# Kernel tuning notes

Measured on AMD Instinct MI355X. Metric: run time of the kernel, lower is better.

The kernel has to match this reference:

```python
import jax, jax.numpy as jnp
import numpy as np

IMG = 448; P = 16; C = 3; D = 512; DC = 8; DS = 4
NH = IMG // P            # 28 patches per side
NPATCH = NH * NH         # 784
PDIM = C * P * P         # 768
BATCH = 32
EPS = 1e-5


def setup_inputs() -> dict:
    key = jax.random.key(0)
    ks = jax.random.split(key, 10)
    def lin(k, fan_in, shape):
        bound = 1.0 / np.sqrt(fan_in)
        return jax.random.uniform(k, shape, jnp.float32, -bound, bound)
    return {
        "images": jax.random.normal(ks[0], (BATCH, C, IMG, IMG), jnp.float32),
        "W_patch": lin(ks[1], PDIM, (PDIM, D)),
        "b_patch": jnp.zeros((D,), jnp.float32),
        "pos_embed": jax.random.normal(ks[2], (1, NPATCH, D), jnp.float32) * 0.02,
        "W_coord": lin(ks[3], D, (D, DC)),
        "b_coord": jnp.zeros((DC,), jnp.float32),
        "W_spinor": lin(ks[4], D, (D, DS)),
        "b_spinor": jnp.zeros((DS,), jnp.float32),
        "W_embed": lin(ks[5], DC, (DC, D)),
        "b_embed": jnp.zeros((D,), jnp.float32),
        "ln_gamma": jnp.ones((D,), jnp.float32),
        "ln_beta": jnp.zeros((D,), jnp.float32),
        "W_out": lin(ks[6], D, (D, D)),
        "b_out": jnp.zeros((D,), jnp.float32),
    }


def reference(images, W_patch, b_patch, pos_embed, W_coord, b_coord,
              W_spinor, b_spinor, W_embed, b_embed,
              ln_gamma, ln_beta, W_out, b_out):
    B = images.shape[0]
    # patchify == F.unfold(kernel=stride=P).transpose(1,2):
    # patches[b, bh*NH+bw, c*P*P + i*P + j] = images[b, c, bh*P+i, bw*P+j]
    patches = images.reshape(B, C, NH, P, NH, P)
    patches = patches.transpose(0, 2, 4, 1, 3, 5).reshape(B, NPATCH, PDIM)
    # patch embed + positional embedding  -> (B, NPATCH, D)
    x = patches @ W_patch + b_patch + pos_embed
    # manifold projection: coords (B,N,DC), spinor (B,N,DS)
    coords = x @ W_coord + b_coord
    spinor = x @ W_spinor + b_spinor
    # K0 scalar bilinear: psi^T psi -> (B, N)
    K0 = jnp.sum(spinor * spinor, axis=-1)
    # embed back from manifold coords -> (B, N, D)
    x_manifold = coords @ W_embed + b_embed
    # K0-modulated remix + residual
    x_enh = x_manifold * K0[..., None] + x
    # output projection: LayerNorm -> Linear
    mu = jnp.mean(x_enh, axis=-1, keepdims=True)
    var = jnp.mean(jnp.square(x_enh - mu), axis=-1, keepdims=True)
    x_norm = (x_enh - mu) * jax.lax.rsqrt(var + EPS) * ln_gamma + ln_beta
    return x_norm @ W_out + b_out
```

## Files before the change

### kernel.cpp

```cpp
#include <hip/hip_runtime.h>
#include <hip/hip_bf16.h>
#include <stdint.h>


typedef __bf16 bf16_t;
typedef bf16_t bf16x8 __attribute__((ext_vector_type(8)));
typedef bf16_t bf16x4 __attribute__((ext_vector_type(4)));
typedef float  f32x4  __attribute__((ext_vector_type(4)));

#define IMG     448
#define PSZ     16
#define NHP     28
#define NPATCH  784
#define PDIM    768
#define DMODEL  512
#define MROWS   25088

__device__ __forceinline__ void gload16(void* lds, const void* g) {
  __builtin_amdgcn_global_load_lds(
      (__attribute__((address_space(1))) void*)(uintptr_t)g,
      (__attribute__((address_space(3))) void*)lds,
      16, 0, 0);
}

__global__ __launch_bounds__(256) void transpose_to_bf16(
    const float* __restrict__ src, bf16_t* __restrict__ dst, int K, int N)
{
  __shared__ float t[64][65];
  const int tx = threadIdx.x;
  const int ty = threadIdx.y;
  const int bx = blockIdx.x * 64;
  const int by = blockIdx.y * 64;
  #pragma unroll
  for (int r = ty; r < 64; r += 4)
    t[r][tx] = src[(size_t)(by + r) * N + (bx + tx)];
  __syncthreads();
  #pragma unroll
  for (int r = ty; r < 64; r += 4)
    dst[(size_t)(bx + r) * K + (by + tx)] = (bf16_t)t[tx][r];
}

__global__ __launch_bounds__(256) void manifold_prep(
    const float* __restrict__ Wc, const float* __restrict__ Ws,
    bf16_t* __restrict__ Wcsg)
{
  const int idx = blockIdx.x * 256 + threadIdx.x;
  if (idx < 8192) {
    const int r = idx >> 9, n = idx & 511;
    float v = 0.f;
    if (r < 8)       v = Wc[n * 8 + r];
    else if (r < 12) v = Ws[n * 4 + (r - 8)];
    Wcsg[idx] = (bf16_t)v;
  }
}

__global__ __launch_bounds__(256) void gemm1_fused(
    const float* __restrict__ images, const bf16_t* __restrict__ BT,
    const float* __restrict__ bias, const float* __restrict__ pos,
    bf16_t* __restrict__ outp)
{
  __shared__ bf16_t As[64 * 64];
  __shared__ bf16_t Bs[128 * 64];
  constexpr int NT = PDIM / 64;

  const int tid  = threadIdx.x;
  const int orig = blockIdx.x;
  const int wg   = (orig & 7) * 196 + (orig >> 3);
  const int n0   = (wg & 3) * 128;
  const int m0   = (wg >> 2) * 64;

  const int wave = tid >> 6, lane = tid & 63;

  const int r_loc = tid >> 2;
  const int seg   = tid & 3;
  {
  }
  const int m  = m0 + r_loc;
  const int b  = m / NPATCH;
  const int p  = m - b * NPATCH;
  const int ph = p / NHP;
  const int pw = p - ph * NHP;
  const float* abase = images + ((size_t)(b * 3) * IMG + ph * PSZ) * IMG + pw * PSZ;
  bf16_t* aw0 = As + r_loc * 64 + (((2 * seg)     ^ (r_loc & 7)) * 8);
  bf16_t* aw1 = As + r_loc * 64 + (((2 * seg + 1) ^ (r_loc & 7)) * 8);

  const int ra = lane >> 3;
  const int ca = (lane & 7) ^ ra;
  const bf16_t* bg = BT + (size_t)(n0 + wave * 8 + ra) * PDIM + ca * 8;
  bf16_t* bl0 = Bs + (wave * 8) * 64;
  bf16_t* bl1 = Bs + (wave * 8 + 32) * 64;
  bf16_t* bl2 = Bs + (wave * 8 + 64) * 64;
  bf16_t* bl3 = Bs + (wave * 8 + 96) * 64;

  const int wm = (wave >> 1) * 32;
  const int wn = (wave & 1) * 64;
  const int lr = lane & 15;
  const int lt = lane >> 4;

  f32x4 acc[2][4] = {};

  for (int t = 0; t < NT; ++t) {
    const int k0 = t * 64;
    const float* asrc = abase + (size_t)(t >> 2) * (IMG * IMG)
                              + ((t & 3) * 4 + seg) * IMG;
    const float4 v0 = *(const float4*)(asrc + 0);
    const float4 v1 = *(const float4*)(asrc + 4);
    const float4 v2 = *(const float4*)(asrc + 8);
    const float4 v3 = *(const float4*)(asrc + 12);

    __syncthreads();
    bf16x8 w0, w1;
    w0[0] = (bf16_t)v0.x; w0[1] = (bf16_t)v0.y; w0[2] = (bf16_t)v0.z; w0[3] = (bf16_t)v0.w;
    w0[4] = (bf16_t)v1.x; w0[5] = (bf16_t)v1.y; w0[6] = (bf16_t)v1.z; w0[7] = (bf16_t)v1.w;
    w1[0] = (bf16_t)v2.x; w1[1] = (bf16_t)v2.y; w1[2] = (bf16_t)v2.z; w1[3] = (bf16_t)v2.w;
    w1[4] = (bf16_t)v3.x; w1[5] = (bf16_t)v3.y; w1[6] = (bf16_t)v3.z; w1[7] = (bf16_t)v3.w;
    *(bf16x8*)aw0 = w0;
    *(bf16x8*)aw1 = w1;
    gload16(bl0, bg + k0);
    gload16(bl1, bg + 32 * PDIM + k0);
    gload16(bl2, bg + 64 * PDIM + k0);
    gload16(bl3, bg + 96 * PDIM + k0);
    __syncthreads();

    #pragma unroll
    for (int ks = 0; ks < 2; ++ks) {
      const int c = ks * 4 + lt;
      bf16x8 af[2], bfr[4];
      #pragma unroll
      for (int i = 0; i < 2; ++i) {
        const int row = wm + i * 16 + lr;
        af[i] = *(const bf16x8*)&As[row * 64 + ((c ^ (row & 7)) * 8)];
      }
      #pragma unroll
      for (int j = 0; j < 4; ++j) {
        const int row = wn + j * 16 + lr;
        bfr[j] = *(const bf16x8*)&Bs[row * 64 + ((c ^ (row & 7)) * 8)];
      }
      #pragma unroll
      for (int i = 0; i < 2; ++i)
        #pragma unroll
        for (int j = 0; j < 4; ++j)
          acc[i][j] = __builtin_amdgcn_mfma_f32_16x16x32_bf16(af[i], bfr[j], acc[i][j], 0, 0, 0);
    }
  }

  const int q4 = lt << 2;
  const int colb = n0 + wn;
  #pragma unroll
  for (int i = 0; i < 2; ++i) {
    #pragma unroll
    for (int r = 0; r < 4; ++r) {
      const int mm = m0 + wm + i * 16 + q4 + r;
      const int pp = mm % NPATCH;
      const float* pe = pos + (size_t)pp * DMODEL;
      bf16_t* orow = outp + (size_t)mm * DMODEL;
      #pragma unroll
      for (int j = 0; j < 4; ++j) {
        const int nn = colb + j * 16 + lr;
        orow[nn] = (bf16_t)(acc[i][j][r] + bias[nn] + pe[nn]);
      }
    }
  }
}

__global__ __launch_bounds__(256) void gemm2_v5(
    const bf16_t* __restrict__ A, const bf16_t* __restrict__ BT,
    const float* __restrict__ bias, float* __restrict__ outp)
{
  __shared__ bf16_t As[64 * 64];
  __shared__ bf16_t Bs[128 * 64];
  constexpr int KDIM = DMODEL;
  constexpr int NT = KDIM / 64;

  const int tid  = threadIdx.x;
  const int orig = blockIdx.x;
  const int wg   = (orig & 7) * 196 + (orig >> 3);
  const int n0   = (wg & 3) * 128;
  const int m0   = (wg >> 2) * 64;

  const int wave = tid >> 6, lane = tid & 63;
  const int ra = lane >> 3;
  const int ca = (lane & 7) ^ ra;
  const bf16_t* ag = A  + (size_t)(m0 + wave * 8 + ra) * KDIM + ca * 8;
  const bf16_t* bg = BT + (size_t)(n0 + wave * 8 + ra) * KDIM + ca * 8;
  bf16_t* al0 = As + (wave * 8) * 64;
  bf16_t* al1 = As + (wave * 8 + 32) * 64;
  bf16_t* bl0 = Bs + (wave * 8) * 64;
  bf16_t* bl1 = Bs + (wave * 8 + 32) * 64;
  bf16_t* bl2 = Bs + (wave * 8 + 64) * 64;
  bf16_t* bl3 = Bs + (wave * 8 + 96) * 64;

  const int wm = (wave >> 1) * 32;
  const int wn = (wave & 1) * 64;
  const int lr = lane & 15;
  const int lt = lane >> 4;

  f32x4 acc[2][4] = {};

  for (int t = 0; t < NT; ++t) {
    const int k0 = t * 64;
    __syncthreads();
    gload16(al0, ag + k0);
    gload16(al1, ag + 32 * KDIM + k0);
    gload16(bl0, bg + k0);
    gload16(bl1, bg + 32 * KDIM + k0);
    gload16(bl2, bg + 64 * KDIM + k0);
    gload16(bl3, bg + 96 * KDIM + k0);
    __syncthreads();

    #pragma unroll
    for (int ks = 0; ks < 2; ++ks) {
      const int c = ks * 4 + lt;
      bf16x8 af[2], bfr[4];
      #pragma unroll
      for (int i = 0; i < 2; ++i) {
        const int row = wm + i * 16 + lr;
        af[i] = *(const bf16x8*)&As[row * 64 + ((c ^ (row & 7)) * 8)];
      }
      #pragma unroll
      for (int j = 0; j < 4; ++j) {
        const int row = wn + j * 16 + lr;
        bfr[j] = *(const bf16x8*)&Bs[row * 64 + ((c ^ (row & 7)) * 8)];
      }
      #pragma unroll
      for (int i = 0; i < 2; ++i)
        #pragma unroll
        for (int j = 0; j < 4; ++j)
          acc[i][j] = __builtin_amdgcn_mfma_f32_16x16x32_bf16(af[i], bfr[j], acc[i][j], 0, 0, 0);
    }
  }

  const int q4 = lt << 2;
  const int colb = n0 + wn;
  #pragma unroll
  for (int i = 0; i < 2; ++i) {
    #pragma unroll
    for (int r = 0; r < 4; ++r) {
      const int mm = m0 + wm + i * 16 + q4 + r;
      float* orow = outp + (size_t)mm * DMODEL;
      #pragma unroll
      for (int j = 0; j < 4; ++j) {
        const int nn = colb + j * 16 + lr;
        orow[nn] = acc[i][j][r] + bias[nn];
      }
    }
  }
}

__global__ __launch_bounds__(64) void manifold_v5(
    bf16_t* __restrict__ x, const bf16_t* __restrict__ Wcsg,
    const float* __restrict__ b_coord, const float* __restrict__ b_spinor,
    const float* __restrict__ We, const float* __restrict__ be,
    const float* __restrict__ gamma, const float* __restrict__ beta)
{
  __shared__ float cbuf[16][12];

  const int lane = threadIdx.x;
  const int lr   = lane & 15;
  const int lk   = (lane >> 4) << 3;
  const int q4   = (lane >> 4) << 2;
  const int m0w  = blockIdx.x * 16;

  float bbv[4];
  #pragma unroll
  for (int r = 0; r < 4; ++r) {
    if (q4 == 0)      bbv[r] = b_coord[r];
    else if (q4 == 4) bbv[r] = b_coord[4 + r];
    else if (q4 == 8) bbv[r] = b_spinor[r];
    else              bbv[r] = 0.f;
  }

  const bf16_t* xrow = x + (size_t)(m0w + lr) * DMODEL + lk;
  const bf16_t* wrow = Wcsg + lr * DMODEL + lk;
  f32x4 acc1 = {0.f, 0.f, 0.f, 0.f};
  #pragma unroll
  for (int ks = 0; ks < 16; ++ks) {
    const bf16x8 bf = *(const bf16x8*)(xrow + ks * 32);
    const bf16x8 wf = *(const bf16x8*)(wrow + ks * 32);
    acc1 = __builtin_amdgcn_mfma_f32_16x16x32_bf16(wf, bf, acc1, 0, 0, 0);
  }
  float sv[4];
  #pragma unroll
  for (int r = 0; r < 4; ++r) sv[r] = acc1[r] + bbv[r];

  if (q4 == 8) {
    cbuf[lr][8] = sv[0] * sv[0] + sv[1] * sv[1] + sv[2] * sv[2] + sv[3] * sv[3];
  } else if (q4 == 0 || q4 == 4) {
    f32x4 st = {sv[0], sv[1], sv[2], sv[3]};
    *(f32x4*)&cbuf[lr][q4] = st;
  }
  __syncthreads();

  const int n0 = lane * 8;
  f32x4 wlo[8], whi[8];
  #pragma unroll
  for (int dc = 0; dc < 8; ++dc) {
    wlo[dc] = *(const f32x4*)&We[dc * DMODEL + n0];
    whi[dc] = *(const f32x4*)&We[dc * DMODEL + n0 + 4];
  }
  const f32x4 beL = *(const f32x4*)&be[n0];
  const f32x4 beH = *(const f32x4*)&be[n0 + 4];
  const f32x4 gL  = *(const f32x4*)&gamma[n0];
  const f32x4 gH  = *(const f32x4*)&gamma[n0 + 4];
  const f32x4 btL = *(const f32x4*)&beta[n0];
  const f32x4 btH = *(const f32x4*)&beta[n0 + 4];

  #pragma unroll 2
  for (int rr = 0; rr < 16; ++rr) {
    const size_t row = (size_t)m0w + rr;
    const bf16x8 xv = *(const bf16x8*)(x + row * DMODEL + n0);
    const f32x4 c0 = *(const f32x4*)&cbuf[rr][0];
    const f32x4 c1 = *(const f32x4*)&cbuf[rr][4];
    const float k0 = cbuf[rr][8];

    float v[8];
    float s1 = 0.f, s2 = 0.f;
    #pragma unroll
    for (int e = 0; e < 4; ++e) {
      float xm = beL[e];
      #pragma unroll
      for (int dc = 0; dc < 4; ++dc) xm += c0[dc] * wlo[dc][e];
      #pragma unroll
      for (int dc = 0; dc < 4; ++dc) xm += c1[dc] * wlo[4 + dc][e];
      const float vv = xm * k0 + (float)xv[e];
      v[e] = vv; s1 += vv; s2 += vv * vv;
    }
    #pragma unroll
    for (int e = 0; e < 4; ++e) {
      float xm = beH[e];
      #pragma unroll
      for (int dc = 0; dc < 4; ++dc) xm += c0[dc] * whi[dc][e];
      #pragma unroll
      for (int dc = 0; dc < 4; ++dc) xm += c1[dc] * whi[4 + dc][e];
      const float vv = xm * k0 + (float)xv[4 + e];
      v[4 + e] = vv; s1 += vv; s2 += vv * vv;
    }

    #pragma unroll
    for (int off = 1; off <= 32; off <<= 1) {
      s1 += __shfl_xor(s1, off, 64);
      s2 += __shfl_xor(s2, off, 64);
    }
    const float mu  = s1 * (1.f / 512.f);
    const float var = s2 * (1.f / 512.f) - mu * mu;
    const float rs  = rsqrtf(var + 1e-5f);

    bf16x8 o;
    #pragma unroll
    for (int e = 0; e < 4; ++e) {
      o[e]     = (bf16_t)((v[e]     - mu) * rs * gL[e] + btL[e]);
      o[4 + e] = (bf16_t)((v[4 + e] - mu) * rs * gH[e] + btH[e]);
    }
    *(bf16x8*)(x + row * DMODEL + n0) = o;
  }
}

extern "C" void kernel_launch(void* const* d_in, const int* in_sizes, int n_in,
                              void* d_out, int out_size, void* d_ws, size_t ws_size,
                              hipStream_t stream)
{
  const float* images    = (const float*)d_in[0];
  const float* W_patch   = (const float*)d_in[1];
  const float* b_patch   = (const float*)d_in[2];
  const float* pos_embed = (const float*)d_in[3];
  const float* W_coord   = (const float*)d_in[4];
  const float* b_coord   = (const float*)d_in[5];
  const float* W_spinor  = (const float*)d_in[6];
  const float* b_spinor  = (const float*)d_in[7];
  const float* W_embed   = (const float*)d_in[8];
  const float* b_embed   = (const float*)d_in[9];
  const float* ln_gamma  = (const float*)d_in[10];
  const float* ln_beta   = (const float*)d_in[11];
  const float* W_out     = (const float*)d_in[12];
  const float* b_out     = (const float*)d_in[13];
  float* out = (float*)d_out;

  const size_t SZ_X    = (size_t)MROWS * DMODEL * 2;
  const size_t SZ_WPT  = (size_t)DMODEL * PDIM * 2;
  const size_t SZ_WOT  = (size_t)DMODEL * DMODEL * 2;

  char* ws = (char*)d_ws;
  char* p  = ws;
  bf16_t* x    = (bf16_t*)p;   p += SZ_X;
  bf16_t* WpT  = (bf16_t*)p;   p += SZ_WPT;
  bf16_t* WoT  = (bf16_t*)p;   p += SZ_WOT;
  bf16_t* Wcsg = (bf16_t*)p;

  hipLaunchKernelGGL(transpose_to_bf16, dim3(8, 12), dim3(64, 4), 0, stream,
                     W_patch, WpT, PDIM, DMODEL);
  hipLaunchKernelGGL(transpose_to_bf16, dim3(8, 8), dim3(64, 4), 0, stream,
                     W_out, WoT, DMODEL, DMODEL);
  hipLaunchKernelGGL(manifold_prep, dim3(32), dim3(256), 0, stream,
                     W_coord, W_spinor, Wcsg);

  hipLaunchKernelGGL(gemm1_fused, dim3(1568), dim3(256), 0, stream,
                     images, WpT, b_patch, pos_embed, x);

  hipLaunchKernelGGL(manifold_v5, dim3(MROWS / 16), dim3(64), 0, stream,
                     x, Wcsg, b_coord, b_spinor, W_embed, b_embed, ln_gamma, ln_beta);

  hipLaunchKernelGGL(gemm2_v5, dim3(1568), dim3(256), 0, stream,
                     x, WoT, b_out, out);
}
```

Baseline: 123.3 us.

## Split patchify into separate kernel and triple-buffer GEMM LDS loads

Moves the fp32-to-bf16 patch extraction out of the first GEMM into a standalone patchify kernel that writes a bf16 patch matrix. Both GEMMs then share one templated kernel with a three-stage LDS ring buffer of async global-to-LDS loads, two tiles in flight, waited on with explicit vmcnt counts, so memory latency overlaps MFMA work. The cost is an extra pass that writes and rereads a large intermediate patch buffer, plus triple the LDS per block, which may lower occupancy.

```diff
diff --git a/kernel.cpp b/kernel.cpp
--- a/kernel.cpp
+++ b/kernel.cpp
@@ -54,14 +54,47 @@
   }
 }
 
-__global__ __launch_bounds__(256) void gemm1_fused(
-    const float* __restrict__ images, const bf16_t* __restrict__ BT,
+__global__ __launch_bounds__(256) void patchify_bf16(
+    const float* __restrict__ images, bf16_t* __restrict__ Apat)
+{
+  __shared__ bf16_t t[16][456];
+  const int tid = threadIdx.x;
+  const int bid = blockIdx.x;
+  const int b = bid / 84, rem = bid % 84;
+  const int c = rem / 28, ph = rem % 28;
+  const float* src = images + ((size_t)(b * 3 + c) * IMG + ph * PSZ) * IMG;
+
+  #pragma unroll
+  for (int idx = tid; idx < 16 * 112; idx += 256) {
+    const int i = idx / 112, x4 = idx % 112;
+    const float4 v = *(const float4*)(src + (size_t)i * IMG + x4 * 4);
+    bf16x4 w;
+    w[0] = (bf16_t)v.x; w[1] = (bf16_t)v.y; w[2] = (bf16_t)v.z; w[3] = (bf16_t)v.w;
+    *(bf16x4*)&t[i][x4 * 4] = w;
+  }
+  __syncthreads();
+
+  const size_t mbase = (size_t)b * NPATCH + (size_t)ph * NHP;
+  #pragma unroll
+  for (int idx = tid; idx < 28 * 64; idx += 256) {
+    const int pw = idx >> 6, e = idx & 63;
+    const int i = e >> 2, j4 = e & 3;
+    const bf16x4 w = *(const bf16x4*)&t[i][pw * 16 + j4 * 4];
+    *(bf16x4*)&Apat[(mbase + pw) * PDIM + c * 256 + i * 16 + j4 * 4] = w;
+  }
+}
+
+template<int KDIM, int EPI>
+__global__ __launch_bounds__(256) void gemm_bf16(
+    const bf16_t* __restrict__ A, const bf16_t* __restrict__ BT,
     const float* __restrict__ bias, const float* __restrict__ pos,
-    bf16_t* __restrict__ outp)
-{
-  __shared__ bf16_t As[64 * 64];
-  __shared__ bf16_t Bs[128 * 64];
-  constexpr int NT = PDIM / 64;
+    void* __restrict__ outp)
+{
+  __shared__ bf16_t As[3 * 64 * 64];
+  __shared__ bf16_t Bs[3 * 128 * 64];
+  constexpr int ABUF = 64 * 64;
+  constexpr int BBUF = 128 * 64;
+  constexpr int NT = KDIM / 64;
 
   const int tid  = threadIdx.x;
   const int orig = blockIdx.x;
@@ -71,57 +104,44 @@
 
   const int wave = tid >> 6, lane = tid & 63;
 
-  const int r_loc = tid >> 2;
-  const int seg   = tid & 3;
-  {
-  }
-  const int m  = m0 + r_loc;
-  const int b  = m / NPATCH;
-  const int p  = m - b * NPATCH;
-  const int ph = p / NHP;
-  const int pw = p - ph * NHP;
-  const float* abase = images + ((size_t)(b * 3) * IMG + ph * PSZ) * IMG + pw * PSZ;
-  bf16_t* aw0 = As + r_loc * 64 + (((2 * seg)     ^ (r_loc & 7)) * 8);
-  bf16_t* aw1 = As + r_loc * 64 + (((2 * seg + 1) ^ (r_loc & 7)) * 8);
-
   const int ra = lane >> 3;
   const int ca = (lane & 7) ^ ra;
-  const bf16_t* bg = BT + (size_t)(n0 + wave * 8 + ra) * PDIM + ca * 8;
-  bf16_t* bl0 = Bs + (wave * 8) * 64;
-  bf16_t* bl1 = Bs + (wave * 8 + 32) * 64;
-  bf16_t* bl2 = Bs + (wave * 8 + 64) * 64;
-  bf16_t* bl3 = Bs + (wave * 8 + 96) * 64;
+  const bf16_t* ag = A  + (size_t)(m0 + wave * 8 + ra) * KDIM + ca * 8;
+  const bf16_t* bg = BT + (size_t)(n0 + wave * 8 + ra) * KDIM + ca * 8;
+  const int aoff0 = (wave * 8) * 64;
+  const int aoff1 = (wave * 8 + 32) * 64;
+  const int boff0 = (wave * 8) * 64;
+  const int boff1 = (wave * 8 + 32) * 64;
+  const int boff2 = (wave * 8 + 64) * 64;
+  const int boff3 = (wave * 8 + 96) * 64;
 
   const int wm = (wave >> 1) * 32;
   const int wn = (wave & 1) * 64;
   const int lr = lane & 15;
   const int lt = lane >> 4;
 
+  auto STAGE = [&](int buf, int k0) {
+    gload16(As + buf * ABUF + aoff0, ag + k0);
+    gload16(As + buf * ABUF + aoff1, ag + 32 * KDIM + k0);
+    gload16(Bs + buf * BBUF + boff0, bg + k0);
+    gload16(Bs + buf * BBUF + boff1, bg + 32 * KDIM + k0);
+    gload16(Bs + buf * BBUF + boff2, bg + 64 * KDIM + k0);
+    gload16(Bs + buf * BBUF + boff3, bg + 96 * KDIM + k0);
+  };
+
+  STAGE(0, 0);
+  STAGE(1, 64);
+
   f32x4 acc[2][4] = {};
 
   for (int t = 0; t < NT; ++t) {
-    const int k0 = t * 64;
-    const float* asrc = abase + (size_t)(t >> 2) * (IMG * IMG)
-                              + ((t & 3) * 4 + seg) * IMG;
-    const float4 v0 = *(const float4*)(asrc + 0);
-    const float4 v1 = *(const float4*)(asrc + 4);
-    const float4 v2 = *(const float4*)(asrc + 8);
-    const float4 v3 = *(const float4*)(asrc + 12);
-
-    __syncthreads();
-    bf16x8 w0, w1;
-    w0[0] = (bf16_t)v0.x; w0[1] = (bf16_t)v0.y; w0[2] = (bf16_t)v0.z; w0[3] = (bf16_t)v0.w;
-    w0[4] = (bf16_t)v1.x; w0[5] = (bf16_t)v1.y; w0[6] = (bf16_t)v1.z; w0[7] = (bf16_t)v1.w;
-    w1[0] = (bf16_t)v2.x; w1[1] = (bf16_t)v2.y; w1[2] = (bf16_t)v2.z; w1[3] = (bf16_t)v2.w;
-    w1[4] = (bf16_t)v3.x; w1[5] = (bf16_t)v3.y; w1[6] = (bf16_t)v3.z; w1[7] = (bf16_t)v3.w;
-    *(bf16x8*)aw0 = w0;
-    *(bf16x8*)aw1 = w1;
-    gload16(bl0, bg + k0);
-    gload16(bl1, bg + 32 * PDIM + k0);
-    gload16(bl2, bg + 64 * PDIM + k0);
-    gload16(bl3, bg + 96 * PDIM + k0);
-    __syncthreads();
-
+    if (t < NT - 1) asm volatile("s_waitcnt vmcnt(6)" ::: "memory");
+    else            asm volatile("s_waitcnt vmcnt(0)" ::: "memory");
+    __builtin_amdgcn_s_barrier();
+    if (t + 2 < NT) STAGE((t + 2) % 3, (t + 2) * 64);
+
+    const bf16_t* Ab = As + (t % 3) * ABUF;
+    const bf16_t* Bb = Bs + (t % 3) * BBUF;
     #pragma unroll
     for (int ks = 0; ks < 2; ++ks) {
       const int c = ks * 4 + lt;
@@ -129,12 +149,12 @@
       #pragma unroll
       for (int i = 0; i < 2; ++i) {
         const int row = wm + i * 16 + lr;
-        af[i] = *(const bf16x8*)&As[row * 64 + ((c ^ (row & 7)) * 8)];
+        af[i] = *(const bf16x8*)&Ab[row * 64 + ((c ^ (row & 7)) * 8)];
       }
       #pragma unroll
       for (int j = 0; j < 4; ++j) {
         const int row = wn + j * 16 + lr;
-        bfr[j] = *(const bf16x8*)&Bs[row * 64 + ((c ^ (row & 7)) * 8)];
+        bfr[j] = *(const bf16x8*)&Bb[row * 64 + ((c ^ (row & 7)) * 8)];
       }
       #pragma unroll
       for (int i = 0; i < 2; ++i)
@@ -151,97 +171,22 @@
     #pragma unroll
     for (int r = 0; r < 4; ++r) {
       const int mm = m0 + wm + i * 16 + q4 + r;
-      const int pp = mm % NPATCH;
-      const float* pe = pos + (size_t)pp * DMODEL;
-      bf16_t* orow = outp + (size_t)mm * DMODEL;
-      #pragma unroll
-      for (int j = 0; j < 4; ++j) {
-        const int nn = colb + j * 16 + lr;
-        orow[nn] = (bf16_t)(acc[i][j][r] + bias[nn] + pe[nn]);
-      }
-    }
-  }
-}
-
-__global__ __launch_bounds__(256) void gemm2_v5(
-    const bf16_t* __restrict__ A, const bf16_t* __restrict__ BT,
-    const float* __restrict__ bias, float* __restrict__ outp)
-{
-  __shared__ bf16_t As[64 * 64];
-  __shared__ bf16_t Bs[128 * 64];
-  constexpr int KDIM = DMODEL;
-  constexpr int NT = KDIM / 64;
-
-  const int tid  = threadIdx.x;
-  const int orig = blockIdx.x;
-  const int wg   = (orig & 7) * 196 + (orig >> 3);
-  const int n0   = (wg & 3) * 128;
-  const int m0   = (wg >> 2) * 64;
-
-  const int wave = tid >> 6, lane = tid & 63;
-  const int ra = lane >> 3;
-  const int ca = (lane & 7) ^ ra;
-  const bf16_t* ag = A  + (size_t)(m0 + wave * 8 + ra) * KDIM + ca * 8;
-  const bf16_t* bg = BT + (size_t)(n0 + wave * 8 + ra) * KDIM + ca * 8;
-  bf16_t* al0 = As + (wave * 8) * 64;
-  bf16_t* al1 = As + (wave * 8 + 32) * 64;
-  bf16_t* bl0 = Bs + (wave * 8) * 64;
-  bf16_t* bl1 = Bs + (wave * 8 + 32) * 64;
-  bf16_t* bl2 = Bs + (wave * 8 + 64) * 64;
-  bf16_t* bl3 = Bs + (wave * 8 + 96) * 64;
-
-  const int wm = (wave >> 1) * 32;
-  const int wn = (wave & 1) * 64;
-  const int lr = lane & 15;
-  const int lt = lane >> 4;
-
-  f32x4 acc[2][4] = {};
-
-  for (int t = 0; t < NT; ++t) {
-    const int k0 = t * 64;
-    __syncthreads();
-    gload16(al0, ag + k0);
-    gload16(al1, ag + 32 * KDIM + k0);
-    gload16(bl0, bg + k0);
-    gload16(bl1, bg + 32 * KDIM + k0);
-    gload16(bl2, bg + 64 * KDIM + k0);
-    gload16(bl3, bg + 96 * KDIM + k0);
-    __syncthreads();
-
-    #pragma unroll
-    for (int ks = 0; ks < 2; ++ks) {
-      const int c = ks * 4 + lt;
-      bf16x8 af[2], bfr[4];
-      #pragma unroll
-      for (int i = 0; i < 2; ++i) {
-        const int row = wm + i * 16 + lr;
-        af[i] = *(const bf16x8*)&As[row * 64 + ((c ^ (row & 7)) * 8)];
-      }
-      #pragma unroll
-      for (int j = 0; j < 4; ++j) {
-        const int row = wn + j * 16 + lr;
-        bfr[j] = *(const bf16x8*)&Bs[row * 64 + ((c ^ (row & 7)) * 8)];
-      }
-      #pragma unroll
-      for (int i = 0; i < 2; ++i)
+      if (EPI == 0) {
+        const int pp = mm % NPATCH;
+        const float* pe = pos + (size_t)pp * DMODEL;
+        bf16_t* orow = (bf16_t*)outp + (size_t)mm * DMODEL;
         #pragma unroll
-        for (int j = 0; j < 4; ++j)
-          acc[i][j] = __builtin_amdgcn_mfma_f32_16x16x32_bf16(af[i], bfr[j], acc[i][j], 0, 0, 0);
-    }
-  }
-
-  const int q4 = lt << 2;
-  const int colb = n0 + wn;
-  #pragma unroll
-  for (int i = 0; i < 2; ++i) {
-    #pragma unroll
-    for (int r = 0; r < 4; ++r) {
-      const int mm = m0 + wm + i * 16 + q4 + r;
-      float* orow = outp + (size_t)mm * DMODEL;
-      #pragma unroll
-      for (int j = 0; j < 4; ++j) {
-        const int nn = colb + j * 16 + lr;
-        orow[nn] = acc[i][j][r] + bias[nn];
+        for (int j = 0; j < 4; ++j) {
+          const int nn = colb + j * 16 + lr;
+          orow[nn] = (bf16_t)(acc[i][j][r] + bias[nn] + pe[nn]);
+        }
+      } else {
+        float* orow = (float*)outp + (size_t)mm * DMODEL;
+        #pragma unroll
+        for (int j = 0; j < 4; ++j) {
+          const int nn = colb + j * 16 + lr;
+          orow[nn] = acc[i][j][r] + bias[nn];
+        }
       }
     }
   }
@@ -375,12 +320,14 @@
   const float* b_out     = (const float*)d_in[13];
   float* out = (float*)d_out;
 
+  const size_t SZ_APAT = (size_t)MROWS * PDIM * 2;
   const size_t SZ_X    = (size_t)MROWS * DMODEL * 2;
   const size_t SZ_WPT  = (size_t)DMODEL * PDIM * 2;
   const size_t SZ_WOT  = (size_t)DMODEL * DMODEL * 2;
 
   char* ws = (char*)d_ws;
   char* p  = ws;
+  bf16_t* Apat = (bf16_t*)p;   p += SZ_APAT;
   bf16_t* x    = (bf16_t*)p;   p += SZ_X;
   bf16_t* WpT  = (bf16_t*)p;   p += SZ_WPT;
   bf16_t* WoT  = (bf16_t*)p;   p += SZ_WOT;
@@ -393,12 +340,14 @@
   hipLaunchKernelGGL(manifold_prep, dim3(32), dim3(256), 0, stream,
                      W_coord, W_spinor, Wcsg);
 
-  hipLaunchKernelGGL(gemm1_fused, dim3(1568), dim3(256), 0, stream,
-                     images, WpT, b_patch, pos_embed, x);
+  hipLaunchKernelGGL(patchify_bf16, dim3(32 * 3 * 28), dim3(256), 0, stream,
+                     images, Apat);
+  hipLaunchKernelGGL((gemm_bf16<PDIM, 0>), dim3(1568), dim3(256), 0, stream,
+                     Apat, WpT, b_patch, pos_embed, (void*)x);
 
   hipLaunchKernelGGL(manifold_v5, dim3(MROWS / 16), dim3(64), 0, stream,
                      x, Wcsg, b_coord, b_spinor, W_embed, b_embed, ln_gamma, ln_beta);
 
-  hipLaunchKernelGGL(gemm2_v5, dim3(1568), dim3(256), 0, stream,
-                     x, WoT, b_out, out);
-}
+  hipLaunchKernelGGL((gemm_bf16<DMODEL, 1>), dim3(1568), dim3(256), 0, stream,
+                     x, WoT, b_out, (const float*)nullptr, (void*)out);
+}
```

Measured after the change: 118.5 us. 1.04x faster.
